# Kernel tuning notes

Measured on AMD Instinct MI355X. Metric: run time of the kernel, lower is better.

The kernel has to match this reference:

```python
import jax, jax.numpy as jnp
import numpy as np

N = 100000   # nodes
E = 1600000  # edges
D = 128      # input feature dim
H = 64       # hidden dim
G = 64       # graphs in batch


def setup_inputs() -> dict:
    key = jax.random.key(0)
    ks = jax.random.split(key, 12)
    x = jax.random.normal(ks[0], (N, D), dtype=jnp.float32)
    ei = jax.random.randint(ks[1], (2, E), 0, N, dtype=jnp.int32)
    ew = jax.random.uniform(ks[2], (E,), dtype=jnp.float32)
    b = jnp.sort(jax.random.randint(ks[3], (N,), 0, G, dtype=jnp.int32))
    s = 0.05
    W1 = jax.random.normal(ks[4], (D, H), jnp.float32) * s
    b1 = jnp.zeros((H,), jnp.float32)
    W2 = jax.random.normal(ks[5], (H, H), jnp.float32) * s
    b2 = jnp.zeros((H,), jnp.float32)
    Wm1 = jax.random.normal(ks[6], (H, 32), jnp.float32) * s
    bm1 = jnp.zeros((32,), jnp.float32)
    Wm2 = jax.random.normal(ks[7], (32, 1), jnp.float32) * s
    bm2 = jnp.zeros((1,), jnp.float32)
    return {"x": x, "ei": ei, "ew": ew, "b": b,
            "W1": W1, "b1": b1, "W2": W2, "b2": b2,
            "Wm1": Wm1, "bm1": bm1, "Wm2": Wm2, "bm2": bm2}


def _gcn_norm(ei, ew, n):
    # PyG gcn_norm with add_self_loops=True (self-loop weight 1)
    loops = jnp.arange(n, dtype=ei.dtype)
    row = jnp.concatenate([ei[0], loops])
    col = jnp.concatenate([ei[1], loops])
    w = jnp.concatenate([ew, jnp.ones((n,), ew.dtype)])
    deg = jax.ops.segment_sum(w, col, num_segments=n)
    dinv = jnp.where(deg > 0, jax.lax.rsqrt(deg), 0.0)
    norm = dinv[row] * w * dinv[col]  # [E+N]
    return row, col, norm


def _gcn_conv(x, W, bias, row, col, norm, n):
    h = x @ W                                   # [N,H] small GEMM
    msg = h[row] * norm[:, None]                # gather over edges
    return jax.ops.segment_sum(msg, col, num_segments=n) + bias


def reference(x, ei, ew, b, W1, b1, W2, b2, Wm1, bm1, Wm2, bm2):
    n = x.shape[0]
    row, col, norm = _gcn_norm(ei, ew, n)
    h = jax.nn.relu(_gcn_conv(x, W1, b1, row, col, norm, n))
    h = jax.nn.relu(_gcn_conv(h, W2, b2, row, col, norm, n))
    # global_mean_pool over batch vector b
    sums = jax.ops.segment_sum(h, b, num_segments=G)
    cnt = jax.ops.segment_sum(jnp.ones((n,), h.dtype), b, num_segments=G)
    pooled = sums / jnp.maximum(cnt, 1.0)[:, None]  # [G,H]
    # MLP head: Linear(H,32) -> ReLU -> Linear(32,1)
    return jax.nn.relu(pooled @ Wm1 + bm1) @ Wm2 + bm2
```

## Files before the change

### kernel.cpp

```cpp
#include <hip/hip_runtime.h>
#include <hip/hip_bf16.h>
#include <hip/hip_fp16.h>


#define DIMH 64
#define BSH 7
#define BSZ 128
#define NBUCK_MAX 1024
#define EPB 4096
#define ESTRIDE 3072
#define CSTRIDE 4096

__global__ __launch_bounds__(256) void k_initcur(int* cursor, int nbuck) {
    int i = blockIdx.x * 256 + threadIdx.x;
    if (i < nbuck) cursor[i] = i * ESTRIDE;
}

__global__ __launch_bounds__(512) void k_part(const int* __restrict__ row,
                                              const int* __restrict__ col,
                                              const float* __restrict__ ew,
                                              int* __restrict__ cursor,
                                              unsigned long long* __restrict__ part,
                                              int E, int nbuck) {
    __shared__ int h[NBUCK_MAX];
    __shared__ int h2[NBUCK_MAX];
    __shared__ int st[NBUCK_MAX];
    for (int i = threadIdx.x; i < nbuck; i += 512) { h[i] = 0; h2[i] = 0; }
    __syncthreads();
    int ebeg = blockIdx.x * EPB;
    int eend = min(ebeg + EPB, E);
    for (int e = ebeg + threadIdx.x; e < eend; e += 512)
        atomicAdd(&h[col[e] >> BSH], 1);
    __syncthreads();
    for (int i = threadIdx.x; i < nbuck; i += 512) {
        int c = h[i];
        st[i] = c ? atomicAdd(&cursor[i], c) : 0;
    }
    __syncthreads();
    for (int e = ebeg + threadIdx.x; e < eend; e += 512) {
        int c = col[e];
        int b = c >> BSH;
        int r = atomicAdd(&h2[b], 1);
        int slot = st[b] + r;
        if (slot < (b + 1) * ESTRIDE) {
            unsigned long long rec =
                ((unsigned long long)__float_as_uint(ew[e]) << 32) |
                ((unsigned long long)(unsigned)row[e] << 8) |
                (unsigned)(c & (BSZ - 1));
            part[slot] = rec;
        }
    }
}

__global__ __launch_bounds__(256) void k_sortB(const unsigned long long* __restrict__ part,
                                               const int* __restrict__ cursor,
                                               int2* __restrict__ csr,
                                               unsigned* __restrict__ rp,
                                               float* __restrict__ dinv, int N) {
    __shared__ int cnt[BSZ];
    __shared__ int scn[BSZ];
    __shared__ int cur[BSZ];
    __shared__ float dg[BSZ];
    int b = blockIdx.x;
    int nb0 = b << BSH;
    int nn = min(BSZ, N - nb0);
    int tid = threadIdx.x;
    if (tid < BSZ) { cnt[tid] = 0; dg[tid] = 1.0f; }
    __syncthreads();
    int ebeg = b * ESTRIDE;
    int eend = min(cursor[b], (b + 1) * ESTRIDE);
    for (int e = ebeg + tid; e < eend; e += 256)
        atomicAdd(&cnt[(int)(part[e] & (BSZ - 1))], 1);
    __syncthreads();
    int pc = 0;
    if (tid < BSZ) pc = min((cnt[tid] + 7) & ~7, 504);
    if (tid < BSZ) scn[tid] = pc;
    __syncthreads();
    for (int o = 1; o < BSZ; o <<= 1) {
        int t = 0;
        if (tid >= o && tid < BSZ) t = scn[tid - o];
        __syncthreads();
        if (tid >= o && tid < BSZ) scn[tid] += t;
        __syncthreads();
    }
    int Pb = b * CSTRIDE;
    int pofs = 0;
    if (tid < BSZ) {
        pofs = scn[tid] - pc;
        cur[tid] = pofs;
        if (tid < nn)
            rp[nb0 + tid] = ((unsigned)(pc >> 3) << 26) | (unsigned)(Pb + pofs);
    }
    __syncthreads();
    for (int e = ebeg + tid; e < eend; e += 256) {
        unsigned long long rec = part[e];
        int cl = (int)(rec & (BSZ - 1));
        float w = __uint_as_float((unsigned)(rec >> 32));
        int slot = atomicAdd(&cur[cl], 1);
        csr[Pb + slot] = make_int2((int)((rec >> 8) & 0xFFFFFF), __float_as_int(w));
        atomicAdd(&dg[cl], w);
    }
    __syncthreads();
    if (tid < nn) {
        int c = min(cnt[tid], pc);
        for (int k = c; k < pc; k++)
            csr[Pb + pofs + k] = make_int2(nb0 + tid, 0);
        dinv[nb0 + tid] = rsqrtf(dg[tid]);
    }
}

template <int K, int H>
__global__ __launch_bounds__(256) void k_gemm_f32(const float* __restrict__ X,
                                                  const float* __restrict__ W,
                                                  const float* __restrict__ dinv,
                                                  __half* __restrict__ Y, int n) {
    __shared__ float Ws[K * H];
    int tid = threadIdx.x;
    for (int i = tid * 4; i < K * H; i += 256 * 4)
        *(float4*)&Ws[i] = *(const float4*)&W[i];
    __syncthreads();

    constexpr int TPR = H / 16;
    constexpr int RPT = 4;
    int c0 = (tid % TPR) * 16;
    int rg = tid / TPR;
    int row0 = blockIdx.x * ((256 / TPR) * RPT) + rg * RPT;
    if (row0 >= n) return;

    float acc[RPT][16];
#pragma unroll
    for (int r = 0; r < RPT; r++)
#pragma unroll
        for (int j = 0; j < 16; j++) acc[r][j] = 0.f;

    int ridx[RPT];
#pragma unroll
    for (int r = 0; r < RPT; r++) ridx[r] = min(row0 + r, n - 1);

    for (int k = 0; k < K; k += 4) {
        float4 xv[RPT];
#pragma unroll
        for (int r = 0; r < RPT; r++)
            xv[r] = *(const float4*)&X[(size_t)ridx[r] * K + k];
#pragma unroll
        for (int kk = 0; kk < 4; kk++) {
            const float* wp = &Ws[(k + kk) * H + c0];
            float w[16];
#pragma unroll
            for (int j = 0; j < 16; j++) w[j] = wp[j];
#pragma unroll
            for (int r = 0; r < RPT; r++) {
                float xs = (&xv[r].x)[kk];
#pragma unroll
                for (int j = 0; j < 16; j++) acc[r][j] += xs * w[j];
            }
        }
    }
#pragma unroll
    for (int r = 0; r < RPT; r++) {
        if (row0 + r < n) {
            float di = dinv[row0 + r];
            __half hb[16];
#pragma unroll
            for (int j = 0; j < 16; j++) hb[j] = __float2half(di * acc[r][j]);
            __half* yr = Y + (size_t)(row0 + r) * H + c0;
            *(uint4*)&yr[0] = *(uint4*)&hb[0];
            *(uint4*)&yr[8] = *(uint4*)&hb[8];
        }
    }
}

template <int K, int H>
__global__ __launch_bounds__(256) void k_gemm_f16(const __half* __restrict__ X,
                                                  const float* __restrict__ W,
                                                  const float* __restrict__ dinv,
                                                  __half* __restrict__ Y, int n) {
    __shared__ float Ws[K * H];
    int tid = threadIdx.x;
    for (int i = tid * 4; i < K * H; i += 256 * 4)
        *(float4*)&Ws[i] = *(const float4*)&W[i];
    __syncthreads();

    constexpr int TPR = H / 16;
    constexpr int RPT = 4;
    int c0 = (tid % TPR) * 16;
    int rg = tid / TPR;
    int row0 = blockIdx.x * ((256 / TPR) * RPT) + rg * RPT;
    if (row0 >= n) return;

    float acc[RPT][16];
#pragma unroll
    for (int r = 0; r < RPT; r++)
#pragma unroll
        for (int j = 0; j < 16; j++) acc[r][j] = 0.f;

    int ridx[RPT];
#pragma unroll
    for (int r = 0; r < RPT; r++) ridx[r] = min(row0 + r, n - 1);

    for (int k = 0; k < K; k += 8) {
        uint4 raw[RPT];
#pragma unroll
        for (int r = 0; r < RPT; r++)
            raw[r] = *(const uint4*)&X[(size_t)ridx[r] * K + k];
#pragma unroll
        for (int kk = 0; kk < 8; kk++) {
            const float* wp = &Ws[(k + kk) * H + c0];
            float w[16];
#pragma unroll
            for (int j = 0; j < 16; j++) w[j] = wp[j];
#pragma unroll
            for (int r = 0; r < RPT; r++) {
                __half xh = ((const __half*)&raw[r])[kk];
                float xs = __half2float(xh);
#pragma unroll
                for (int j = 0; j < 16; j++) acc[r][j] += xs * w[j];
            }
        }
    }
#pragma unroll
    for (int r = 0; r < RPT; r++) {
        if (row0 + r < n) {
            float di = dinv[row0 + r];
            __half hb[16];
#pragma unroll
            for (int j = 0; j < 16; j++) hb[j] = __float2half(di * acc[r][j]);
            __half* yr = Y + (size_t)(row0 + r) * H + c0;
            *(uint4*)&yr[0] = *(uint4*)&hb[0];
            *(uint4*)&yr[8] = *(uint4*)&hb[8];
        }
    }
}

__global__ __launch_bounds__(256) void k_aggN(const __half* __restrict__ Hin,
                                              const unsigned* __restrict__ rp,
                                              const int2* __restrict__ csr,
                                              const float* __restrict__ dinv,
                                              const float* __restrict__ bias,
                                              __half* __restrict__ Hout, int n) {
    int lane = threadIdx.x & 63;
    int wv = threadIdx.x >> 6;
    int node = blockIdx.x * 4 + wv;
    if (node >= n) return;
    unsigned pk = rp[node];
    int p = (int)(pk & 0x3FFFFFFu);
    int iters = (int)(pk >> 26);
    int fp = lane & 31;
    bool hi = lane >= 32;
    const unsigned* HinU = (const unsigned*)Hin;
    float ax = 0.f, ay = 0.f;
    if (!hi) {
        unsigned su = HinU[(size_t)node * 32 + fp];
        float2 sf = __half22float2(*(__half2*)&su);
        ax = sf.x; ay = sf.y;
    }
    for (int it = 0; it < iters; it++, p += 8) {
        int4 m0 = *(const int4*)&csr[p];
        int4 m1 = *(const int4*)&csr[p + 2];
        int4 m2 = *(const int4*)&csr[p + 4];
        int4 m3 = *(const int4*)&csr[p + 6];
        int   s0 = hi ? m0.z : m0.x;
        float w0 = __int_as_float(hi ? m0.w : m0.y);
        int   s1 = hi ? m1.z : m1.x;
        float w1 = __int_as_float(hi ? m1.w : m1.y);
        int   s2 = hi ? m2.z : m2.x;
        float w2 = __int_as_float(hi ? m2.w : m2.y);
        int   s3 = hi ? m3.z : m3.x;
        float w3 = __int_as_float(hi ? m3.w : m3.y);
        unsigned u0 = HinU[(size_t)s0 * 32 + fp];
        unsigned u1 = HinU[(size_t)s1 * 32 + fp];
        unsigned u2 = HinU[(size_t)s2 * 32 + fp];
        unsigned u3 = HinU[(size_t)s3 * 32 + fp];
        float2 f0 = __half22float2(*(__half2*)&u0);
        float2 f1 = __half22float2(*(__half2*)&u1);
        float2 f2 = __half22float2(*(__half2*)&u2);
        float2 f3 = __half22float2(*(__half2*)&u3);
        ax += w0 * f0.x; ay += w0 * f0.y;
        ax += w1 * f1.x; ay += w1 * f1.y;
        ax += w2 * f2.x; ay += w2 * f2.y;
        ax += w3 * f3.x; ay += w3 * f3.y;
    }
    ax += __shfl_xor(ax, 32, 64);
    ay += __shfl_xor(ay, 32, 64);
    if (!hi) {
        float di = dinv[node];
        float vx = di * ax + bias[2 * fp];
        float vy = di * ay + bias[2 * fp + 1];
        vx = vx > 0.f ? vx : 0.f;
        vy = vy > 0.f ? vy : 0.f;
        __half2 o = __floats2half2_rn(vx, vy);
        *(__half2*)&Hout[(size_t)node * DIMH + 2 * fp] = o;
    }
}

__global__ __launch_bounds__(256) void k_pool(const __half* __restrict__ Hin,
                                              const int* __restrict__ b,
                                              float* __restrict__ sums,
                                              float* __restrict__ cntG, int n) {
    const int CHUNK = 64;
    int lane = threadIdx.x & 63;
    int wave = threadIdx.x >> 6;
    int start = (blockIdx.x * 4 + wave) * CHUNK;
    if (start >= n) return;
    int end = min(start + CHUNK, n);
    float acc = 0.f;
    int g_cur = b[start];
    int cnt_local = 0;
    for (int i = start; i < end; i++) {
        int g = b[i];
        if (g != g_cur) {
            atomicAdd(&sums[g_cur * DIMH + lane], acc);
            if (lane == 0) atomicAdd(&cntG[g_cur], (float)cnt_local);
            acc = 0.f;
            cnt_local = 0;
            g_cur = g;
        }
        acc += __half2float(Hin[(size_t)i * DIMH + lane]);
        cnt_local++;
    }
    atomicAdd(&sums[g_cur * DIMH + lane], acc);
    if (lane == 0) atomicAdd(&cntG[g_cur], (float)cnt_local);
}

__global__ __launch_bounds__(64) void k_mlp(const float* __restrict__ sums,
                                            const float* __restrict__ cntG,
                                            const float* __restrict__ Wm1,
                                            const float* __restrict__ bm1,
                                            const float* __restrict__ Wm2,
                                            const float* __restrict__ bm2,
                                            float* __restrict__ out, int G) {
    int g = threadIdx.x;
    if (g >= G) return;
    float c = cntG[g];
    float inv = 1.f / (c > 1.f ? c : 1.f);
    float pooled[DIMH];
#pragma unroll
    for (int k = 0; k < DIMH; k++) pooled[k] = sums[g * DIMH + k] * inv;
    float o = 0.f;
    for (int j = 0; j < 32; j++) {
        float t = bm1[j];
#pragma unroll
        for (int k = 0; k < DIMH; k++) t += pooled[k] * Wm1[k * 32 + j];
        t = t > 0.f ? t : 0.f;
        o += t * Wm2[j];
    }
    out[g] = o + bm2[0];
}


extern "C" void kernel_launch(void* const* d_in, const int* in_sizes, int n_in,
                              void* d_out, int out_size, void* d_ws, size_t ws_size,
                              hipStream_t stream) {
    const float* x   = (const float*)d_in[0];
    const int*   ei  = (const int*)d_in[1];
    const float* ew  = (const float*)d_in[2];
    const int*   bvec= (const int*)d_in[3];
    const float* W1  = (const float*)d_in[4];
    const float* b1  = (const float*)d_in[5];
    const float* W2  = (const float*)d_in[6];
    const float* b2  = (const float*)d_in[7];
    const float* Wm1 = (const float*)d_in[8];
    const float* bm1 = (const float*)d_in[9];
    const float* Wm2 = (const float*)d_in[10];
    const float* bm2 = (const float*)d_in[11];
    float* out = (float*)d_out;

    const int E = in_sizes[2];
    const int N = in_sizes[3];
    const int G = out_size;
    const int* row = ei;
    const int* col = ei + E;
    const int nbuck = (N + BSZ - 1) >> BSH;

    char* p = (char*)d_ws;
    auto alloc = [&](size_t bytes) {
        void* r = (void*)p;
        p += (bytes + 255) & ~(size_t)255;
        return r;
    };

    unsigned long long* part = (unsigned long long*)alloc((size_t)nbuck * ESTRIDE * 8);
    int2*  csr    = (int2*)alloc((size_t)nbuck * CSTRIDE * 8);
    int*   cursor = (int*)alloc((size_t)nbuck * 4);
    unsigned* rp  = (unsigned*)alloc((size_t)N * 4);
    float* dinv   = (float*)alloc((size_t)N * 4);
    __half* hA    = (__half*)alloc((size_t)N * DIMH * 2);
    __half* hB    = (__half*)alloc((size_t)N * DIMH * 2);
    int zeroInts  = G * DIMH + G;
    float* sums   = (float*)alloc((size_t)zeroInts * 4);
    float* cntG   = sums + G * DIMH;

    hipMemsetAsync(sums, 0, (size_t)zeroInts * 4, stream);

    const int PB = (E + EPB - 1) / EPB;

    k_initcur<<<(nbuck + 255) / 256, 256, 0, stream>>>(cursor, nbuck);
    k_part<<<PB, 512, 0, stream>>>(row, col, ew, cursor, part, E, nbuck);
    k_sortB<<<nbuck, 256, 0, stream>>>(part, cursor, csr, rp, dinv, N);

    k_gemm_f32<128, DIMH><<<(N + 255) / 256, 256, 0, stream>>>(x, W1, dinv, hA, N);
    k_aggN<<<(N + 3) / 4, 256, 0, stream>>>(hA, rp, csr, dinv, b1, hB, N);

    k_gemm_f16<DIMH, DIMH><<<(N + 255) / 256, 256, 0, stream>>>(hB, W2, dinv, hA, N);
    k_aggN<<<(N + 3) / 4, 256, 0, stream>>>(hA, rp, csr, dinv, b2, hB, N);

    k_pool<<<(N + 255) / 256, 256, 0, stream>>>(hB, bvec, sums, cntG, N);
    k_mlp<<<1, 64, 0, stream>>>(sums, cntG, Wm1, bm1, Wm2, bm2, out, G);
}
```

Baseline: 361.1 us.

## Fuse layer-1 aggregation with layer-2 GEMM and drop cursor init kernel

Layer-1 aggregation, bias and ReLU now feed straight into the 64x64 W2 transform in one persistent kernel. Each wave stages its node's hidden vector in shared memory and computes the projected row, so the separate GEMM kernel and the round trip of the intermediate through global memory go away. The cursor array now starts at zero through the existing memset, and the bucket base offset is added inside the partition and sort kernels, which removes the init kernel launch. The cost is a 16KB W2 tile loaded per block and a per-node 64-wide dot product inside the gather loop, which may lower occupancy.

```diff
diff --git a/kernel.cpp b/kernel.cpp
--- a/kernel.cpp
+++ b/kernel.cpp
@@ -10,11 +10,6 @@
 #define EPB 4096
 #define ESTRIDE 3072
 #define CSTRIDE 4096
-
-__global__ __launch_bounds__(256) void k_initcur(int* cursor, int nbuck) {
-    int i = blockIdx.x * 256 + threadIdx.x;
-    if (i < nbuck) cursor[i] = i * ESTRIDE;
-}
 
 __global__ __launch_bounds__(512) void k_part(const int* __restrict__ row,
                                               const int* __restrict__ col,
@@ -34,7 +29,7 @@
     __syncthreads();
     for (int i = threadIdx.x; i < nbuck; i += 512) {
         int c = h[i];
-        st[i] = c ? atomicAdd(&cursor[i], c) : 0;
+        st[i] = c ? i * ESTRIDE + atomicAdd(&cursor[i], c) : 0;
     }
     __syncthreads();
     for (int e = ebeg + threadIdx.x; e < eend; e += 512) {
@@ -68,7 +63,7 @@
     if (tid < BSZ) { cnt[tid] = 0; dg[tid] = 1.0f; }
     __syncthreads();
     int ebeg = b * ESTRIDE;
-    int eend = min(cursor[b], (b + 1) * ESTRIDE);
+    int eend = ebeg + min(cursor[b], ESTRIDE);
     for (int e = ebeg + tid; e < eend; e += 256)
         atomicAdd(&cnt[(int)(part[e] & (BSZ - 1))], 1);
     __syncthreads();
@@ -170,65 +165,92 @@
     }
 }
 
-template <int K, int H>
-__global__ __launch_bounds__(256) void k_gemm_f16(const __half* __restrict__ X,
-                                                  const float* __restrict__ W,
-                                                  const float* __restrict__ dinv,
-                                                  __half* __restrict__ Y, int n) {
-    __shared__ float Ws[K * H];
+__global__ __launch_bounds__(256) void k_agg1f(const __half* __restrict__ Hin,
+                                               const unsigned* __restrict__ rp,
+                                               const int2* __restrict__ csr,
+                                               const float* __restrict__ dinv,
+                                               const float* __restrict__ bias,
+                                               const float* __restrict__ W2,
+                                               __half* __restrict__ T2, int n) {
+    __shared__ float W2s[DIMH * DIMH];
+    __shared__ unsigned hbuf[4][32];
     int tid = threadIdx.x;
-    for (int i = tid * 4; i < K * H; i += 256 * 4)
-        *(float4*)&Ws[i] = *(const float4*)&W[i];
-    __syncthreads();
-
-    constexpr int TPR = H / 16;
-    constexpr int RPT = 4;
-    int c0 = (tid % TPR) * 16;
-    int rg = tid / TPR;
-    int row0 = blockIdx.x * ((256 / TPR) * RPT) + rg * RPT;
-    if (row0 >= n) return;
-
-    float acc[RPT][16];
-#pragma unroll
-    for (int r = 0; r < RPT; r++)
-#pragma unroll
-        for (int j = 0; j < 16; j++) acc[r][j] = 0.f;
-
-    int ridx[RPT];
-#pragma unroll
-    for (int r = 0; r < RPT; r++) ridx[r] = min(row0 + r, n - 1);
-
-    for (int k = 0; k < K; k += 8) {
-        uint4 raw[RPT];
-#pragma unroll
-        for (int r = 0; r < RPT; r++)
-            raw[r] = *(const uint4*)&X[(size_t)ridx[r] * K + k];
-#pragma unroll
-        for (int kk = 0; kk < 8; kk++) {
-            const float* wp = &Ws[(k + kk) * H + c0];
-            float w[16];
-#pragma unroll
-            for (int j = 0; j < 16; j++) w[j] = wp[j];
-#pragma unroll
-            for (int r = 0; r < RPT; r++) {
-                __half xh = ((const __half*)&raw[r])[kk];
-                float xs = __half2float(xh);
-#pragma unroll
-                for (int j = 0; j < 16; j++) acc[r][j] += xs * w[j];
-            }
-        }
-    }
-#pragma unroll
-    for (int r = 0; r < RPT; r++) {
-        if (row0 + r < n) {
-            float di = dinv[row0 + r];
-            __half hb[16];
-#pragma unroll
-            for (int j = 0; j < 16; j++) hb[j] = __float2half(di * acc[r][j]);
-            __half* yr = Y + (size_t)(row0 + r) * H + c0;
-            *(uint4*)&yr[0] = *(uint4*)&hb[0];
-            *(uint4*)&yr[8] = *(uint4*)&hb[8];
-        }
+    for (int i = tid * 4; i < DIMH * DIMH; i += 256 * 4)
+        *(float4*)&W2s[i] = *(const float4*)&W2[i];
+    __syncthreads();
+
+    int lane = tid & 63;
+    int wv = tid >> 6;
+    int fp = lane & 31;
+    bool hi = lane >= 32;
+    const unsigned* HinU = (const unsigned*)Hin;
+    int ngroups = (n + 3) >> 2;
+
+    for (int grp = blockIdx.x; grp < ngroups; grp += gridDim.x) {
+        int node = grp * 4 + wv;
+        if (node >= n) continue;
+        unsigned pk = rp[node];
+        int p = (int)(pk & 0x3FFFFFFu);
+        int iters = (int)(pk >> 26);
+        float ax = 0.f, ay = 0.f;
+        if (!hi) {
+            unsigned su = HinU[(size_t)node * 32 + fp];
+            float2 sf = __half22float2(*(__half2*)&su);
+            ax = sf.x; ay = sf.y;
+        }
+        for (int it = 0; it < iters; it++, p += 8) {
+            int4 m0 = *(const int4*)&csr[p];
+            int4 m1 = *(const int4*)&csr[p + 2];
+            int4 m2 = *(const int4*)&csr[p + 4];
+            int4 m3 = *(const int4*)&csr[p + 6];
+            int   s0 = hi ? m0.z : m0.x;
+            float w0 = __int_as_float(hi ? m0.w : m0.y);
+            int   s1 = hi ? m1.z : m1.x;
+            float w1 = __int_as_float(hi ? m1.w : m1.y);
+            int   s2 = hi ? m2.z : m2.x;
+            float w2 = __int_as_float(hi ? m2.w : m2.y);
+            int   s3 = hi ? m3.z : m3.x;
+            float w3 = __int_as_float(hi ? m3.w : m3.y);
+            unsigned u0 = HinU[(size_t)s0 * 32 + fp];
+            unsigned u1 = HinU[(size_t)s1 * 32 + fp];
+            unsigned u2 = HinU[(size_t)s2 * 32 + fp];
+            unsigned u3 = HinU[(size_t)s3 * 32 + fp];
+            float2 f0 = __half22float2(*(__half2*)&u0);
+            float2 f1 = __half22float2(*(__half2*)&u1);
+            float2 f2 = __half22float2(*(__half2*)&u2);
+            float2 f3 = __half22float2(*(__half2*)&u3);
+            ax += w0 * f0.x; ay += w0 * f0.y;
+            ax += w1 * f1.x; ay += w1 * f1.y;
+            ax += w2 * f2.x; ay += w2 * f2.y;
+            ax += w3 * f3.x; ay += w3 * f3.y;
+        }
+        ax += __shfl_xor(ax, 32, 64);
+        ay += __shfl_xor(ay, 32, 64);
+        float di = dinv[node];
+        if (!hi) {
+            float vx = di * ax + bias[2 * fp];
+            float vy = di * ay + bias[2 * fp + 1];
+            vx = vx > 0.f ? vx : 0.f;
+            vy = vy > 0.f ? vy : 0.f;
+            __half2 hh = __floats2half2_rn(vx, vy);
+            hbuf[wv][fp] = *(unsigned*)&hh;
+        }
+        float acc2 = 0.f;
+        const unsigned* hb = hbuf[wv];
+#pragma unroll
+        for (int k8 = 0; k8 < 8; k8++) {
+            uint4 hc = *(const uint4*)&hb[k8 * 4];
+            float2 g0 = __half22float2(*(__half2*)&hc.x);
+            float2 g1 = __half22float2(*(__half2*)&hc.y);
+            float2 g2 = __half22float2(*(__half2*)&hc.z);
+            float2 g3 = __half22float2(*(__half2*)&hc.w);
+            const float* wc = &W2s[(k8 * 8) * DIMH + lane];
+            acc2 += g0.x * wc[0 * DIMH] + g0.y * wc[1 * DIMH]
+                  + g1.x * wc[2 * DIMH] + g1.y * wc[3 * DIMH]
+                  + g2.x * wc[4 * DIMH] + g2.y * wc[5 * DIMH]
+                  + g3.x * wc[6 * DIMH] + g3.y * wc[7 * DIMH];
+        }
+        T2[(size_t)node * DIMH + lane] = __float2half(di * acc2);
     }
 }
 
@@ -381,29 +403,28 @@
 
     unsigned long long* part = (unsigned long long*)alloc((size_t)nbuck * ESTRIDE * 8);
     int2*  csr    = (int2*)alloc((size_t)nbuck * CSTRIDE * 8);
-    int*   cursor = (int*)alloc((size_t)nbuck * 4);
     unsigned* rp  = (unsigned*)alloc((size_t)N * 4);
     float* dinv   = (float*)alloc((size_t)N * 4);
     __half* hA    = (__half*)alloc((size_t)N * DIMH * 2);
     __half* hB    = (__half*)alloc((size_t)N * DIMH * 2);
-    int zeroInts  = G * DIMH + G;
-    float* sums   = (float*)alloc((size_t)zeroInts * 4);
+    int zeroInts  = nbuck + G * DIMH + G;
+    int* cursor   = (int*)alloc((size_t)zeroInts * 4);
+    float* sums   = (float*)(cursor + nbuck);
     float* cntG   = sums + G * DIMH;
 
-    hipMemsetAsync(sums, 0, (size_t)zeroInts * 4, stream);
+    hipMemsetAsync(cursor, 0, (size_t)zeroInts * 4, stream);
 
     const int PB = (E + EPB - 1) / EPB;
 
-    k_initcur<<<(nbuck + 255) / 256, 256, 0, stream>>>(cursor, nbuck);
     k_part<<<PB, 512, 0, stream>>>(row, col, ew, cursor, part, E, nbuck);
     k_sortB<<<nbuck, 256, 0, stream>>>(part, cursor, csr, rp, dinv, N);
 
     k_gemm_f32<128, DIMH><<<(N + 255) / 256, 256, 0, stream>>>(x, W1, dinv, hA, N);
-    k_aggN<<<(N + 3) / 4, 256, 0, stream>>>(hA, rp, csr, dinv, b1, hB, N);
-
-    k_gemm_f16<DIMH, DIMH><<<(N + 255) / 256, 256, 0, stream>>>(hB, W2, dinv, hA, N);
-    k_aggN<<<(N + 3) / 4, 256, 0, stream>>>(hA, rp, csr, dinv, b2, hB, N);
-
-    k_pool<<<(N + 255) / 256, 256, 0, stream>>>(hB, bvec, sums, cntG, N);
+
+    k_agg1f<<<4096, 256, 0, stream>>>(hA, rp, csr, dinv, b1, W2, hB, N);
+
+    k_aggN<<<(N + 3) / 4, 256, 0, stream>>>(hB, rp, csr, dinv, b2, hA, N);
+
+    k_pool<<<(N + 255) / 256, 256, 0, stream>>>(hA, bvec, sums, cntG, N);
     k_mlp<<<1, 64, 0, stream>>>(sums, cntG, Wm1, bm1, Wm2, bm2, out, G);
 }
```

New measurement: 343.8 us. -4.8%, faster.
